# Optimization experiments

Hardware: AMD Instinct MI355X
Metric: run time of the kernel (lower is better)

Reference implementation:

```python
import jax, jax.numpy as jnp
import numpy as np

EPS = float(np.finfo(np.float32).eps)
NUM_PROP = 5          # config.model.num_prop
NUM_STEP_S2V = 3      # config.model.num_step_set2vec


def _gru_cell(x, h, wih, whh, bih, bhh):
    # PyTorch GRUCell: gate order r, z, n
    gi = x @ wih.T + bih
    gh = h @ whh.T + bhh
    ir, iz, in_ = jnp.split(gi, 3, axis=-1)
    hr, hz, hn = jnp.split(gh, 3, axis=-1)
    r = jax.nn.sigmoid(ir + hr)
    z = jax.nn.sigmoid(iz + hz)
    n = jnp.tanh(in_ + r * hn)
    return (1.0 - z) * n + z * h


def _lstm_cell(x, h, c, wih, whh, bih, bhh):
    # PyTorch LSTMCell: gate order i, f, g, o
    g = x @ wih.T + bih + h @ whh.T + bhh
    i, f, gg, o = jnp.split(g, 4, axis=-1)
    c2 = jax.nn.sigmoid(f) * c + jax.nn.sigmoid(i) * jnp.tanh(gg)
    return jax.nn.sigmoid(o) * jnp.tanh(c2), c2


def _set2vec(m, wih, whh, bih, bhh):
    # Set2Vec / set2set encoder (Vinyals et al. 2015) over a node set m: [N, H].
    # Returns q_star: [2H] = concat(LSTM hidden, attention read).
    H = m.shape[-1]
    h = jnp.zeros((H,), m.dtype)
    c = jnp.zeros((H,), m.dtype)
    q = jnp.zeros((2 * H,), m.dtype)
    for _ in range(NUM_STEP_S2V):
        h, c = _lstm_cell(q, h, c, wih, whh, bih, bhh)
        att = jax.nn.softmax(m @ h)   # [N] attention over set elements
        r = att @ m                   # [H] read vector
        q = jnp.concatenate([h, r])
    return q


def setup_inputs() -> dict:
    key = jax.random.key(0)
    ks = jax.random.split(key, 12)
    B, N, Da, Din, H, E1, Dout = 32, 512, 100, 64, 128, 4, 16
    s = 0.05
    return {
        "node_feat": jax.random.randint(ks[0], (B, N), 0, Da),
        "L": jax.random.randint(ks[1], (B, N, N, E1), 0, 2).astype(jnp.float32),
        "node_emb": jax.random.normal(ks[2], (Da, Din)) * s,
        "W_in": jax.random.normal(ks[3], (H, Din)) * s,
        "b_in": jnp.zeros((H,)),
        "edge_emb": jax.random.normal(ks[4], (E1, H * H)) * s,
        "gru_wih": jax.random.normal(ks[5], (3 * H, E1 * H)) * s,
        "gru_whh": jax.random.normal(ks[6], (3 * H, H)) * s,
        "gru_bih": jnp.zeros((3 * H,)),
        "gru_bhh": jnp.zeros((3 * H,)),
        "lstm_wih": jax.random.normal(ks[7], (4 * H, 2 * H)) * s,
        "lstm_whh": jax.random.normal(ks[8], (4 * H, H)) * s,
        "lstm_bih": jnp.zeros((4 * H,)),
        "lstm_bhh": jnp.zeros((4 * H,)),
        "W_out": jax.random.normal(ks[9], (Dout, 2 * H)) * s,
        "b_out": jnp.zeros((Dout,)),
    }


def reference(node_feat, L, node_emb, W_in, b_in, edge_emb,
              gru_wih, gru_whh, gru_bih, gru_bhh,
              lstm_wih, lstm_whh, lstm_bih, lstm_bhh,
              W_out, b_out):
    B, N = node_feat.shape
    H = W_in.shape[0]
    E1 = edge_emb.shape[0]
    # L[L != 0] = 1.0  (binarize adjacency)
    A = jnp.where(L != 0, 1.0, 0.0).astype(L.dtype)            # [B,N,N,E1]
    # node embedding + input linear
    state = node_emb[node_feat] @ W_in.T + b_in                # [B,N,H]
    Eop = edge_emb.reshape(E1, H, H)                           # per-edge-type operator
    for _ in range(NUM_PROP):
        # per-edge-type message: state @ edge_em  (all types at once)
        msg = jnp.einsum('bnh,ehk->bnek', state, Eop)          # [B,N,E1,H]
        # sum aggregation: bmm(A[...,e], msg_e)
        agg = jnp.einsum('bmne,bnek->bmek', A, msg)            # [B,N,E1,H]
        msg_cat = agg.reshape(B, N, E1 * H)                    # cat over edge types (dim=2)
        state = _gru_cell(msg_cat, state, gru_wih, gru_whh, gru_bih, gru_bhh)
        # dropout p=0.0 -> identity
    # Set2Vec per graph (mask=None path), then output linear
    q = jax.vmap(lambda s: _set2vec(s, lstm_wih, lstm_whh, lstm_bih, lstm_bhh))(state)  # [B,2H]
    return q @ W_out.T + b_out                                 # [B,Dout]
```

## Files before the change

### kernel.cpp

```cpp
#include <hip/hip_runtime.h>
#include <hip/hip_bf16.h>

#define BB 32
#define NN 512
#define DA 100
#define DIN 64
#define HH 128
#define E1 4
#define DOUT 16
#define NPROP 5
#define NS2V 3
#define MHALF 8192

typedef __attribute__((ext_vector_type(8))) short bf16x8;
typedef __attribute__((ext_vector_type(4))) float f32x4;
typedef __attribute__((ext_vector_type(4))) unsigned short us4;
typedef __attribute__((ext_vector_type(8))) unsigned short us8;
typedef unsigned short ushort_t;

__device__ __forceinline__ unsigned short f2bf(float f) {
    __hip_bfloat16 h = __float2bfloat16(f);
    return *reinterpret_cast<unsigned short*>(&h);
}
__device__ __forceinline__ float bf2f(unsigned short u) {
    unsigned v = ((unsigned)u) << 16;
    float f;
    __builtin_memcpy(&f, &v, 4);
    return f;
}

__device__ __forceinline__ void gload_lds16(const void* g, void* l) {
    __builtin_amdgcn_global_load_lds(
        (const __attribute__((address_space(1))) void*)g,
        (__attribute__((address_space(3))) void*)l, 16, 0, 0);
}

__global__ __launch_bounds__(256) void pack_A_kernel(const float* __restrict__ L,
                                                     unsigned* __restrict__ Abits) {
    int t = blockIdx.x * 256 + threadIdx.x;
    int n = t & (NN - 1);
    int m = (t >> 9) & (NN - 1);
    int b = t >> 18;
    float4 v = *reinterpret_cast<const float4*>(L + ((size_t)(b * NN + m) * NN + n) * E1);
    unsigned long long mk[E1];
    mk[0] = __ballot(v.x != 0.f);
    mk[1] = __ballot(v.y != 0.f);
    mk[2] = __ballot(v.z != 0.f);
    mk[3] = __ballot(v.w != 0.f);
    int lane = threadIdx.x & 63;
    if (lane < 8) {
        int e = lane >> 1, half = lane & 1;
        unsigned word = half ? (unsigned)(mk[e] >> 32) : (unsigned)mk[e];
        int wbase = (n >> 5) & ~1;
        Abits[((size_t)(b * E1 + e) * NN + m) * 16 + wbase + half] = word;
    }
}

__global__ void convW_kernel(const float* __restrict__ EE, const float* __restrict__ wih,
                             const float* __restrict__ whh,
                             ushort_t* __restrict__ U_h, ushort_t* __restrict__ U_l,
                             ushort_t* __restrict__ whh_h, ushort_t* __restrict__ whh_l) {
    int t = blockIdx.x * blockDim.x + threadIdx.x;
    if (t < 384 * 512) {
        int col = t & 511;
        int j = t >> 9;
        int e = col >> 7, h = col & 127;
        const float4* wp = reinterpret_cast<const float4*>(wih + (size_t)j * 512 + e * 128);
        const float4* ep = reinterpret_cast<const float4*>(EE + (size_t)e * 16384 + h * 128);
        float acc = 0.f;
        #pragma unroll 8
        for (int k4 = 0; k4 < 32; ++k4) {
            float4 a = wp[k4], b = ep[k4];
            acc = fmaf(a.x, b.x, fmaf(a.y, b.y, fmaf(a.z, b.z, fmaf(a.w, b.w, acc))));
        }
        unsigned short hi = f2bf(acc);
        U_h[t] = hi;
        U_l[t] = f2bf(acc - bf2f(hi));
        return;
    }
    int t2 = t - 384 * 512;
    if (t2 < 384 * 128) {
        float v = whh[t2];
        unsigned short hi = f2bf(v);
        whh_h[t2] = hi;
        whh_l[t2] = f2bf(v - bf2f(hi));
    }
}

__global__ void embed_kernel(const int* __restrict__ nf, const float* __restrict__ emb,
                             const float* __restrict__ Win, const float* __restrict__ bin,
                             ushort_t* __restrict__ s_hi, ushort_t* __restrict__ s_lo) {
    int row = blockIdx.x;
    int h = threadIdx.x;
    __shared__ float e[DIN];
    int a = nf[row];
    if (h < DIN) e[h] = emb[a * DIN + h];
    __syncthreads();
    float acc = bin[h];
    const float* w = Win + h * DIN;
    #pragma unroll
    for (int d = 0; d < DIN; ++d) acc = fmaf(e[d], w[d], acc);
    unsigned short hi = f2bf(acc);
    s_hi[row * HH + h] = hi;
    s_lo[row * HH + h] = f2bf(acc - bf2f(hi));
}

__global__ __launch_bounds__(256) void transpose_kernel(const ushort_t* __restrict__ src,
                                                        ushort_t* __restrict__ dst,
                                                        size_t splane) {
    __shared__ __align__(16) ushort_t tile[128][72];
    int row0 = blockIdx.x * 64;
    int tid = threadIdx.x;
    #pragma unroll
    for (int pl = 0; pl < 2; ++pl) {
        const ushort_t* s = src + pl * splane;
        ushort_t* d = dst + pl * splane;
        #pragma unroll
        for (int q = 0; q < 4; ++q) {
            int idx = q * 256 + tid;
            int r = idx >> 4, h8 = idx & 15;
            bf16x8 v = *reinterpret_cast<const bf16x8*>(s + (size_t)(row0 + r) * HH + h8 * 8);
            #pragma unroll
            for (int j = 0; j < 8; ++j) tile[h8 * 8 + j][r] = (ushort_t)v[j];
        }
        __syncthreads();
        {
            int h = tid >> 1, rseg = (tid & 1) * 32;
            #pragma unroll
            for (int s8 = 0; s8 < 4; ++s8) {
                us8 v = *reinterpret_cast<const us8*>(&tile[h][rseg + s8 * 8]);
                *reinterpret_cast<us8*>(&d[(size_t)h * 16384 + row0 + rseg + s8 * 8]) = v;
            }
        }
        __syncthreads();
    }
}

template <int MODE, bool AGG, bool XBITS, int K, bool XSPLIT, bool WSPLIT>
__global__ __launch_bounds__(256) void mm_kernel(const void* __restrict__ Xp, size_t xplane,
                                                 const ushort_t* __restrict__ W, size_t wplane,
                                                 const float* __restrict__ bias,
                                                 void* __restrict__ outv, size_t oplane,
                                                 int ldx, int ldw, int ldo) {
    __shared__ __align__(16) ushort_t Xs[2][128 * 32];
    __shared__ __align__(16) ushort_t Ws[2][64 * 32];
    int tid = threadIdx.x;
    int row0, col0;
    if constexpr (MODE == 3) {
        row0 = blockIdx.x * 128; col0 = blockIdx.y * 64;
    } else if constexpr (AGG) {
        row0 = (blockIdx.y & 3) * 128; col0 = (blockIdx.y >> 2) * 64;
    } else {
        row0 = blockIdx.y * 128; col0 = blockIdx.x * 64;
    }
    const ushort_t* X = (const ushort_t*)Xp;
    const unsigned* Xb = (const unsigned*)Xp;
    size_t out_off = 0;
    int wko = 0;
    if constexpr (AGG) {
        int bl = blockIdx.x, e = blockIdx.z;
        Xb += (size_t)(bl * E1 + e) * NN * 16;
        wko = bl * NN;
        out_off = (size_t)bl * NN * NN + (size_t)e * HH;
    }
    int lane = tid & 63;
    int wave = tid >> 6;
    int wm = wave & 1, wn = wave >> 1;
    int r16 = lane & 15, kg = lane >> 4;
    int lrow = lane >> 2;
    int lcol = (lane & 3) * 8;

    f32x4 acc[4][2] = {};

    for (int k0 = 0; k0 < K; k0 += 32) {
        unsigned xword;
        if constexpr (XBITS) {
            int m = tid >> 1;
            xword = Xb[(size_t)(row0 + m) * 16 + (k0 >> 5)];
        }
        __syncthreads();
        if constexpr (!XBITS) {
            #pragma unroll
            for (int q2 = 0; q2 < 2; ++q2) {
                int q = wave * 2 + q2;
                const ushort_t* g = X + (size_t)(row0 + q * 16 + lrow) * ldx + k0 + lcol;
                gload_lds16(g, &Xs[0][q * 512]);
                if constexpr (XSPLIT) gload_lds16(g + xplane, &Xs[1][q * 512]);
            }
        } else {
            int m = tid >> 1, sel = tid & 1;
            #pragma unroll
            for (int j8 = 0; j8 < 2; ++j8) {
                bf16x8 xv;
                #pragma unroll
                for (int j = 0; j < 8; ++j)
                    xv[j] = (short)(((xword >> (sel * 16 + j8 * 8 + j)) & 1u) ? 0x3F80 : 0);
                *reinterpret_cast<bf16x8*>(&Xs[0][m * 32 + sel * 16 + j8 * 8]) = xv;
            }
        }
        {
            const ushort_t* g = W + (size_t)(col0 + wave * 16 + lrow) * ldw + wko + k0 + lcol;
            gload_lds16(g, &Ws[0][wave * 512]);
            if constexpr (WSPLIT) gload_lds16(g + wplane, &Ws[1][wave * 512]);
        }
        __syncthreads();
        bf16x8 af_h[4], af_l[4], bf_h[2], bf_l[2];
        #pragma unroll
        for (int mi = 0; mi < 4; ++mi) {
            af_h[mi] = *reinterpret_cast<const bf16x8*>(&Xs[0][(wm * 64 + mi * 16 + r16) * 32 + kg * 8]);
            if constexpr (XSPLIT)
                af_l[mi] = *reinterpret_cast<const bf16x8*>(&Xs[1][(wm * 64 + mi * 16 + r16) * 32 + kg * 8]);
        }
        #pragma unroll
        for (int ni = 0; ni < 2; ++ni) {
            bf_h[ni] = *reinterpret_cast<const bf16x8*>(&Ws[0][(wn * 32 + ni * 16 + r16) * 32 + kg * 8]);
            if constexpr (WSPLIT)
                bf_l[ni] = *reinterpret_cast<const bf16x8*>(&Ws[1][(wn * 32 + ni * 16 + r16) * 32 + kg * 8]);
        }
        #pragma unroll
        for (int mi = 0; mi < 4; ++mi)
            #pragma unroll
            for (int ni = 0; ni < 2; ++ni) {
                acc[mi][ni] = __builtin_amdgcn_mfma_f32_16x16x32_bf16(af_h[mi], bf_h[ni], acc[mi][ni], 0, 0, 0);
                if constexpr (XSPLIT)
                    acc[mi][ni] = __builtin_amdgcn_mfma_f32_16x16x32_bf16(af_l[mi], bf_h[ni], acc[mi][ni], 0, 0, 0);
                if constexpr (WSPLIT)
                    acc[mi][ni] = __builtin_amdgcn_mfma_f32_16x16x32_bf16(af_h[mi], bf_l[ni], acc[mi][ni], 0, 0, 0);
            }
    }

    if constexpr (MODE == 3) {
        float* out = (float*)outv;
        #pragma unroll
        for (int ni = 0; ni < 2; ++ni) {
            int col = col0 + wn * 32 + ni * 16 + r16;
            float bv = bias[col];
            #pragma unroll
            for (int mi = 0; mi < 4; ++mi) {
                int rowb = row0 + wm * 64 + mi * 16 + kg * 4;
                #pragma unroll
                for (int j = 0; j < 4; ++j)
                    out[(size_t)(rowb + j) * ldo + col] = acc[mi][ni][j] + bv;
            }
        }
    } else {
        ushort_t* out = (ushort_t*)outv + out_off;
        #pragma unroll
        for (int ni = 0; ni < 2; ++ni) {
            int col = col0 + wn * 32 + ni * 16 + r16;
            #pragma unroll
            for (int mi = 0; mi < 4; ++mi) {
                int rowb = row0 + wm * 64 + mi * 16 + kg * 4;
                #pragma unroll
                for (int j = 0; j < 4; ++j) {
                    float v = acc[mi][ni][j];
                    unsigned short hv = f2bf(v);
                    out[(size_t)(rowb + j) * ldo + col] = hv;
                    out[oplane + (size_t)(rowb + j) * ldo + col] = f2bf(v - bf2f(hv));
                }
            }
        }
    }
}

__global__ void gru_gate_kernel(const float* __restrict__ gi, const float* __restrict__ gh,
                                ushort_t* __restrict__ s_hi, ushort_t* __restrict__ s_lo,
                                size_t half_off, int total) {
    int t = blockIdx.x * blockDim.x + threadIdx.x;
    if (t >= total) return;
    int row = t >> 7, j = t & 127;
    const float* gir = gi + (size_t)row * 384;
    const float* ghr = gh + (size_t)row * 384;
    float ir = gir[j], iz = gir[128 + j], in_ = gir[256 + j];
    float hr = ghr[j], hz = ghr[128 + j], hn = ghr[256 + j];
    float r = 1.f / (1.f + expf(-(ir + hr)));
    float z = 1.f / (1.f + expf(-(iz + hz)));
    float n = tanhf(in_ + r * hn);
    size_t g = half_off + (size_t)t;
    float h = bf2f(s_hi[g]) + bf2f(s_lo[g]);
    float v = (1.f - z) * n + z * h;
    unsigned short hv = f2bf(v);
    s_hi[g] = hv;
    s_lo[g] = f2bf(v - bf2f(hv));
}


__global__ __launch_bounds__(256) void s2v_g_kernel(int step,
        const float* __restrict__ hvec, const float* __restrict__ rpart,
        const float* __restrict__ wih, const float* __restrict__ whh,
        const float* __restrict__ bih, const float* __restrict__ bhh,
        float* __restrict__ g_all) {
    int b = blockIdx.y, tid = threadIdx.x;
    int j = blockIdx.x * 256 + tid;
    __shared__ float q[256];
    if (step > 0) {
        if (tid < 128) q[tid] = hvec[b * 128 + tid];
        else {
            int h2 = tid - 128;
            const float* rp = rpart + (size_t)b * 512;
            q[tid] = rp[h2] + rp[128 + h2] + rp[256 + h2] + rp[384 + h2];
        }
    } else {
        q[tid] = 0.f;
    }
    __syncthreads();
    float acc = bih[j] + bhh[j];
    if (step > 0) {
        const float4* wi = reinterpret_cast<const float4*>(wih + (size_t)j * 256);
        #pragma unroll 8
        for (int d4 = 0; d4 < 64; ++d4) {
            float4 w = wi[d4];
            acc = fmaf(q[d4 * 4 + 0], w.x, fmaf(q[d4 * 4 + 1], w.y,
                  fmaf(q[d4 * 4 + 2], w.z, fmaf(q[d4 * 4 + 3], w.w, acc))));
        }
        const float4* wp = reinterpret_cast<const float4*>(whh + (size_t)j * 128);
        #pragma unroll 8
        for (int d4 = 0; d4 < 32; ++d4) {
            float4 w = wp[d4];
            acc = fmaf(q[d4 * 4 + 0], w.x, fmaf(q[d4 * 4 + 1], w.y,
                  fmaf(q[d4 * 4 + 2], w.z, fmaf(q[d4 * 4 + 3], w.w, acc))));
        }
    }
    g_all[(size_t)b * 512 + j] = acc;
}

__global__ __launch_bounds__(256) void s2v_cl_kernel(int step,
        const float* __restrict__ g_all, float* __restrict__ cvec, float* __restrict__ hvec,
        const ushort_t* __restrict__ s_hi, const ushort_t* __restrict__ s_lo,
        float* __restrict__ logits) {
    int b = blockIdx.y, chunk = blockIdx.x, tid = threadIdx.x;
    __shared__ float hs[HH];
    if (tid < HH) {
        const float* g = g_all + (size_t)b * 512;
        float i_ = 1.f / (1.f + expf(-g[tid]));
        float f_ = 1.f / (1.f + expf(-g[128 + tid]));
        float g_ = tanhf(g[256 + tid]);
        float o_ = 1.f / (1.f + expf(-g[384 + tid]));
        float c0 = (step == 0) ? 0.f : cvec[b * 128 + tid];
        float c2 = f_ * c0 + i_ * g_;
        float hn = o_ * tanhf(c2);
        hs[tid] = hn;
        if (chunk == 0) { cvec[b * 128 + tid] = c2; hvec[b * 128 + tid] = hn; }
    }
    __syncthreads();
    int n = chunk * 256 + tid;
    const ushort_t* ph = s_hi + ((size_t)b * NN + n) * HH;
    const ushort_t* pl = s_lo + ((size_t)b * NN + n) * HH;
    float lg = 0.f;
    #pragma unroll
    for (int i8 = 0; i8 < 16; ++i8) {
        bf16x8 vh = *reinterpret_cast<const bf16x8*>(ph + i8 * 8);
        bf16x8 vl = *reinterpret_cast<const bf16x8*>(pl + i8 * 8);
        #pragma unroll
        for (int k = 0; k < 8; ++k)
            lg = fmaf(bf2f((ushort_t)vh[k]) + bf2f((ushort_t)vl[k]), hs[i8 * 8 + k], lg);
    }
    logits[(size_t)b * 512 + n] = lg;
}

__global__ __launch_bounds__(256) void s2v_read_kernel(const float* __restrict__ logits,
        const ushort_t* __restrict__ t_hi, const ushort_t* __restrict__ t_lo,
        float* __restrict__ rpart) {
    int b = blockIdx.y, chunk = blockIdx.x, tid = threadIdx.x;
    __shared__ float lgs[NN];
    __shared__ float att[128];
    __shared__ float wred[8];
    __shared__ float red[256];
    lgs[tid] = logits[(size_t)b * 512 + tid];
    lgs[256 + tid] = logits[(size_t)b * 512 + 256 + tid];
    __syncthreads();
    float mv = fmaxf(lgs[tid], lgs[tid + 256]);
    #pragma unroll
    for (int m = 32; m >= 1; m >>= 1) mv = fmaxf(mv, __shfl_xor(mv, m));
    if ((tid & 63) == 0) wred[tid >> 6] = mv;
    __syncthreads();
    float mx = fmaxf(fmaxf(wred[0], wred[1]), fmaxf(wred[2], wred[3]));
    float sv = expf(lgs[tid] - mx) + expf(lgs[tid + 256] - mx);
    #pragma unroll
    for (int m = 32; m >= 1; m >>= 1) sv += __shfl_xor(sv, m);
    if ((tid & 63) == 0) wred[4 + (tid >> 6)] = sv;
    __syncthreads();
    float inv = 1.f / (wred[4] + wred[5] + wred[6] + wred[7]);
    if (tid < 128) att[tid] = expf(lgs[chunk * 128 + tid] - mx) * inv;
    __syncthreads();
    int hh = tid & 127, half = tid >> 7;
    int colb = b * NN + chunk * 128 + half * 64;
    const ushort_t* ph = t_hi + (size_t)hh * 16384 + colb;
    const ushort_t* pl = t_lo + (size_t)hh * 16384 + colb;
    float racc = 0.f;
    #pragma unroll
    for (int i8 = 0; i8 < 8; ++i8) {
        bf16x8 vh = *reinterpret_cast<const bf16x8*>(ph + i8 * 8);
        bf16x8 vl = *reinterpret_cast<const bf16x8*>(pl + i8 * 8);
        #pragma unroll
        for (int k = 0; k < 8; ++k)
            racc = fmaf(att[half * 64 + i8 * 8 + k],
                        bf2f((ushort_t)vh[k]) + bf2f((ushort_t)vl[k]), racc);
    }
    red[tid] = racc;
    __syncthreads();
    if (tid < 128)
        rpart[(size_t)b * 512 + chunk * 128 + tid] = red[tid] + red[128 + tid];
}

__global__ __launch_bounds__(256) void s2v_out_kernel(const float* __restrict__ hvec,
        const float* __restrict__ rpart, const float* __restrict__ Wout,
        const float* __restrict__ bout, float* __restrict__ out) {
    int b = blockIdx.x, tid = threadIdx.x;
    __shared__ float q[256];
    if (tid < 128) q[tid] = hvec[b * 128 + tid];
    else {
        int h2 = tid - 128;
        const float* rp = rpart + (size_t)b * 512;
        q[tid] = rp[h2] + rp[128 + h2] + rp[256 + h2] + rp[384 + h2];
    }
    __syncthreads();
    if (tid < DOUT) {
        float acc = bout[tid];
        const float4* w = reinterpret_cast<const float4*>(Wout + (size_t)tid * 256);
        #pragma unroll 8
        for (int d4 = 0; d4 < 64; ++d4) {
            float4 wv = w[d4];
            acc = fmaf(q[d4 * 4 + 0], wv.x, fmaf(q[d4 * 4 + 1], wv.y,
                  fmaf(q[d4 * 4 + 2], wv.z, fmaf(q[d4 * 4 + 3], wv.w, acc))));
        }
        out[b * DOUT + tid] = acc;
    }
}

extern "C" void kernel_launch(void* const* d_in, const int* in_sizes, int n_in,
                              void* d_out, int out_size, void* d_ws, size_t ws_size,
                              hipStream_t stream) {
    const int*   node_feat = (const int*)d_in[0];
    const float* L         = (const float*)d_in[1];
    const float* node_emb  = (const float*)d_in[2];
    const float* W_in      = (const float*)d_in[3];
    const float* b_in      = (const float*)d_in[4];
    const float* edge_emb  = (const float*)d_in[5];
    const float* gru_wih   = (const float*)d_in[6];
    const float* gru_whh   = (const float*)d_in[7];
    const float* gru_bih   = (const float*)d_in[8];
    const float* gru_bhh   = (const float*)d_in[9];
    const float* lstm_wih  = (const float*)d_in[10];
    const float* lstm_whh  = (const float*)d_in[11];
    const float* lstm_bih  = (const float*)d_in[12];
    const float* lstm_bhh  = (const float*)d_in[13];
    const float* W_out     = (const float*)d_in[14];
    const float* b_out     = (const float*)d_in[15];
    float* out = (float*)d_out;

    char* ws = (char*)d_ws;
    const bool full = ws_size >= ((size_t)110 << 20);

    ushort_t* state_hi  = (ushort_t*)ws;
    ushort_t* stateT_hi = (ushort_t*)(ws + (8u << 20));
    unsigned* Abits     = (unsigned*)(ws + (16u << 20));
    ushort_t* S2        = (ushort_t*)(ws + (20u << 20));
    size_t s2plane      = full ? 8388608u : 4194304u;
    float*    gi        = (float*)(ws + (full ? (52ull << 20) : (36ull << 20)));
    float*    gh        = (float*)(ws + (full ? (76ull << 20) : (48ull << 20)));
    ushort_t* U_h       = (ushort_t*)(ws + (full ? (100ull << 20) : (60ull << 20)));
    ushort_t* U_l       = U_h + 196608;
    ushort_t* whh_h     = U_l + 196608;
    ushort_t* whh_l     = whh_h + 49152;
    float*    s2v       = (float*)(ws + (full ? (101ull << 20) : (61ull << 20)));
    float*    g_all     = s2v;
    float*    logits    = s2v + 16384;
    float*    hvec      = s2v + 32768;
    float*    cvec      = s2v + 36864;
    float*    rpart     = s2v + 40960;

    const size_t SPLANE = 2097152;

    pack_A_kernel<<<(BB * NN * NN) / 256, 256, 0, stream>>>(L, Abits);
    convW_kernel<<<(384 * 512 + 384 * 128) / 256, 256, 0, stream>>>(
        edge_emb, gru_wih, gru_whh, U_h, U_l, whh_h, whh_l);
    embed_kernel<<<BB * NN, 128, 0, stream>>>(node_feat, node_emb, W_in, b_in,
                                              state_hi, state_hi + SPLANE);

    const int nh     = full ? 1 : 2;
    const int graphs = full ? 32 : 16;
    const int ydim   = full ? 128 : 64;
    const int rows   = full ? 16384 : MHALF;

    for (int p = 0; p < NPROP; ++p) {
        transpose_kernel<<<256, 256, 0, stream>>>(state_hi, stateT_hi, SPLANE);
        for (int half = 0; half < nh; ++half) {
            const unsigned* Ab = Abits + (size_t)half * 16 * E1 * NN * 16;
            mm_kernel<4, true, true, 512, false, true><<<dim3(graphs, 8, 4), 256, 0, stream>>>(
                Ab, 0, stateT_hi + (size_t)half * MHALF, SPLANE, nullptr,
                S2, s2plane, 0, 16384, 512);
            mm_kernel<3, false, false, 512, true, true><<<dim3(ydim, 6), 256, 0, stream>>>(
                S2, s2plane, U_h, 196608, gru_bih, gi, 0, 512, 512, 384);
            mm_kernel<3, false, false, 128, true, true><<<dim3(ydim, 6), 256, 0, stream>>>(
                state_hi + (size_t)half * MHALF * HH, SPLANE, whh_h, 49152, gru_bhh,
                gh, 0, 128, 128, 384);
            gru_gate_kernel<<<(rows * HH) / 256, 256, 0, stream>>>(
                gi, gh, state_hi, state_hi + SPLANE,
                (size_t)half * MHALF * HH, rows * HH);
        }
    }
    transpose_kernel<<<256, 256, 0, stream>>>(state_hi, stateT_hi, SPLANE);

    for (int step = 0; step < NS2V; ++step) {
        s2v_g_kernel<<<dim3(2, BB), 256, 0, stream>>>(step, hvec, rpart,
                                                      lstm_wih, lstm_whh, lstm_bih, lstm_bhh,
                                                      g_all);
        s2v_cl_kernel<<<dim3(2, BB), 256, 0, stream>>>(step, g_all, cvec, hvec,
                                                       state_hi, state_hi + SPLANE, logits);
        s2v_read_kernel<<<dim3(4, BB), 256, 0, stream>>>(logits, stateT_hi,
                                                         stateT_hi + SPLANE, rpart);
    }
    s2v_out_kernel<<<BB, 256, 0, stream>>>(hvec, rpart, W_out, b_out, out);
}
```

Measured before the change: 581.1 us.

## Double GEMM K-step to 64 with XOR-swizzled LDS layout

The shared GEMM kernel now stages 64-wide K slices per iteration instead of 32, halving the number of barrier pairs and global-to-LDS rounds. The LDS tiles use an XOR swizzle on 16-byte slots to avoid bank conflicts on the MFMA fragment reads. LDS allocation is sized only for the split planes actually used. It assumes K is a multiple of 64, and the bit-expanded adjacency path now reads one 32-bit word per thread-half.

```diff
diff --git a/kernel.cpp b/kernel.cpp
--- a/kernel.cpp
+++ b/kernel.cpp
@@ -142,8 +142,10 @@
                                                  const float* __restrict__ bias,
                                                  void* __restrict__ outv, size_t oplane,
                                                  int ldx, int ldw, int ldo) {
-    __shared__ __align__(16) ushort_t Xs[2][128 * 32];
-    __shared__ __align__(16) ushort_t Ws[2][64 * 32];
+    constexpr int XP = XSPLIT ? 2 : 1;
+    constexpr int WP = WSPLIT ? 2 : 1;
+    __shared__ __align__(16) ushort_t Xs[XP][128 * 64];
+    __shared__ __align__(16) ushort_t Ws[WP][64 * 64];
     int tid = threadIdx.x;
     int row0, col0;
     if constexpr (MODE == 3) {
@@ -167,66 +169,81 @@
     int wave = tid >> 6;
     int wm = wave & 1, wn = wave >> 1;
     int r16 = lane & 15, kg = lane >> 4;
-    int lrow = lane >> 2;
-    int lcol = (lane & 3) * 8;
+    int lrow = lane >> 3;
+    int lslot = lane & 7;
 
     f32x4 acc[4][2] = {};
 
-    for (int k0 = 0; k0 < K; k0 += 32) {
-        unsigned xword;
+    for (int k0 = 0; k0 < K; k0 += 64) {
+        unsigned xw0;
         if constexpr (XBITS) {
-            int m = tid >> 1;
-            xword = Xb[(size_t)(row0 + m) * 16 + (k0 >> 5)];
+            int m = tid >> 1, sel = tid & 1;
+            xw0 = Xb[(size_t)(row0 + m) * 16 + (k0 >> 5) + sel];
         }
         __syncthreads();
         if constexpr (!XBITS) {
             #pragma unroll
-            for (int q2 = 0; q2 < 2; ++q2) {
-                int q = wave * 2 + q2;
-                const ushort_t* g = X + (size_t)(row0 + q * 16 + lrow) * ldx + k0 + lcol;
+            for (int q2 = 0; q2 < 4; ++q2) {
+                int q = wave * 4 + q2;
+                const ushort_t* g = X + (size_t)(row0 + q * 8 + lrow) * ldx + k0
+                                      + ((lslot ^ lrow) * 8);
                 gload_lds16(g, &Xs[0][q * 512]);
                 if constexpr (XSPLIT) gload_lds16(g + xplane, &Xs[1][q * 512]);
             }
         } else {
             int m = tid >> 1, sel = tid & 1;
             #pragma unroll
-            for (int j8 = 0; j8 < 2; ++j8) {
+            for (int j8 = 0; j8 < 4; ++j8) {
                 bf16x8 xv;
                 #pragma unroll
                 for (int j = 0; j < 8; ++j)
-                    xv[j] = (short)(((xword >> (sel * 16 + j8 * 8 + j)) & 1u) ? 0x3F80 : 0);
-                *reinterpret_cast<bf16x8*>(&Xs[0][m * 32 + sel * 16 + j8 * 8]) = xv;
+                    xv[j] = (short)(((xw0 >> (j8 * 8 + j)) & 1u) ? 0x3F80 : 0);
+                *reinterpret_cast<bf16x8*>(
+                    &Xs[0][m * 64 + (((sel << 2) + j8) ^ (m & 7)) * 8]) = xv;
             }
         }
         {
-            const ushort_t* g = W + (size_t)(col0 + wave * 16 + lrow) * ldw + wko + k0 + lcol;
-            gload_lds16(g, &Ws[0][wave * 512]);
-            if constexpr (WSPLIT) gload_lds16(g + wplane, &Ws[1][wave * 512]);
+            #pragma unroll
+            for (int q2 = 0; q2 < 2; ++q2) {
+                int q = wave * 2 + q2;
+                const ushort_t* g = W + (size_t)(col0 + q * 8 + lrow) * ldw + wko + k0
+                                      + ((lslot ^ lrow) * 8);
+                gload_lds16(g, &Ws[0][q * 512]);
+                if constexpr (WSPLIT) gload_lds16(g + wplane, &Ws[1][q * 512]);
+            }
         }
         __syncthreads();
-        bf16x8 af_h[4], af_l[4], bf_h[2], bf_l[2];
         #pragma unroll
-        for (int mi = 0; mi < 4; ++mi) {
-            af_h[mi] = *reinterpret_cast<const bf16x8*>(&Xs[0][(wm * 64 + mi * 16 + r16) * 32 + kg * 8]);
-            if constexpr (XSPLIT)
-                af_l[mi] = *reinterpret_cast<const bf16x8*>(&Xs[1][(wm * 64 + mi * 16 + r16) * 32 + kg * 8]);
-        }
-        #pragma unroll
-        for (int ni = 0; ni < 2; ++ni) {
-            bf_h[ni] = *reinterpret_cast<const bf16x8*>(&Ws[0][(wn * 32 + ni * 16 + r16) * 32 + kg * 8]);
-            if constexpr (WSPLIT)
-                bf_l[ni] = *reinterpret_cast<const bf16x8*>(&Ws[1][(wn * 32 + ni * 16 + r16) * 32 + kg * 8]);
-        }
-        #pragma unroll
-        for (int mi = 0; mi < 4; ++mi)
+        for (int kk = 0; kk < 2; ++kk) {
+            int sbase = kg + kk * 4;
+            bf16x8 af_h[4], af_l[4], bf_h[2], bf_l[2];
+            #pragma unroll
+            for (int mi = 0; mi < 4; ++mi) {
+                int r = wm * 64 + mi * 16 + r16;
+                int off = r * 64 + (sbase ^ (r & 7)) * 8;
+                af_h[mi] = *reinterpret_cast<const bf16x8*>(&Xs[0][off]);
+                if constexpr (XSPLIT)
+                    af_l[mi] = *reinterpret_cast<const bf16x8*>(&Xs[XP - 1][off]);
+            }
             #pragma unroll
             for (int ni = 0; ni < 2; ++ni) {
-                acc[mi][ni] = __builtin_amdgcn_mfma_f32_16x16x32_bf16(af_h[mi], bf_h[ni], acc[mi][ni], 0, 0, 0);
-                if constexpr (XSPLIT)
-                    acc[mi][ni] = __builtin_amdgcn_mfma_f32_16x16x32_bf16(af_l[mi], bf_h[ni], acc[mi][ni], 0, 0, 0);
+                int r = wn * 32 + ni * 16 + r16;
+                int off = r * 64 + (sbase ^ (r & 7)) * 8;
+                bf_h[ni] = *reinterpret_cast<const bf16x8*>(&Ws[0][off]);
                 if constexpr (WSPLIT)
-                    acc[mi][ni] = __builtin_amdgcn_mfma_f32_16x16x32_bf16(af_h[mi], bf_l[ni], acc[mi][ni], 0, 0, 0);
-            }
+                    bf_l[ni] = *reinterpret_cast<const bf16x8*>(&Ws[WP - 1][off]);
+            }
+            #pragma unroll
+            for (int mi = 0; mi < 4; ++mi)
+                #pragma unroll
+                for (int ni = 0; ni < 2; ++ni) {
+                    acc[mi][ni] = __builtin_amdgcn_mfma_f32_16x16x32_bf16(af_h[mi], bf_h[ni], acc[mi][ni], 0, 0, 0);
+                    if constexpr (XSPLIT)
+                        acc[mi][ni] = __builtin_amdgcn_mfma_f32_16x16x32_bf16(af_l[mi], bf_h[ni], acc[mi][ni], 0, 0, 0);
+                    if constexpr (WSPLIT)
+                        acc[mi][ni] = __builtin_amdgcn_mfma_f32_16x16x32_bf16(af_h[mi], bf_l[ni], acc[mi][ni], 0, 0, 0);
+                }
+        }
     }
 
     if constexpr (MODE == 3) {
```

Measured after the change: 573.5 us (median of 2 runs). About the same (-1.3%).

## Double-buffer LDS tiles in mm_kernel and XOR-swizzle layout to avoid bank conflicts

Applied to the files above, without the earlier changes.

Restructures the GEMM main loop to stage the next K-slice into a second LDS buffer while the current one feeds MFMAs, removing one barrier per iteration and overlapping global-to-LDS loads with compute. It also XOR-swizzles the 8-element column slot by row index on both store and load to reduce LDS bank conflicts on the fragment reads. The cost is double the LDS footprint for split variants, which may lower occupancy. The swizzle must match across the async gload_lds writes and the reads.

```diff
diff --git a/kernel.cpp b/kernel.cpp
--- a/kernel.cpp
+++ b/kernel.cpp
@@ -142,8 +142,10 @@
                                                  const float* __restrict__ bias,
                                                  void* __restrict__ outv, size_t oplane,
                                                  int ldx, int ldw, int ldo) {
-    __shared__ __align__(16) ushort_t Xs[2][128 * 32];
-    __shared__ __align__(16) ushort_t Ws[2][64 * 32];
+    constexpr int XP = XSPLIT ? 2 : 1;
+    constexpr int WP = WSPLIT ? 2 : 1;
+    __shared__ __align__(16) ushort_t Xs[2][XP][128 * 32];
+    __shared__ __align__(16) ushort_t Ws[2][WP][64 * 32];
     int tid = threadIdx.x;
     int row0, col0;
     if constexpr (MODE == 3) {
@@ -168,54 +170,62 @@
     int wm = wave & 1, wn = wave >> 1;
     int r16 = lane & 15, kg = lane >> 4;
     int lrow = lane >> 2;
-    int lcol = (lane & 3) * 8;
+    int lslot = lane & 3;
 
     f32x4 acc[4][2] = {};
 
-    for (int k0 = 0; k0 < K; k0 += 32) {
-        unsigned xword;
-        if constexpr (XBITS) {
-            int m = tid >> 1;
-            xword = Xb[(size_t)(row0 + m) * 16 + (k0 >> 5)];
-        }
-        __syncthreads();
+    auto stage = [&](int buf, int k0) {
         if constexpr (!XBITS) {
             #pragma unroll
             for (int q2 = 0; q2 < 2; ++q2) {
                 int q = wave * 2 + q2;
-                const ushort_t* g = X + (size_t)(row0 + q * 16 + lrow) * ldx + k0 + lcol;
-                gload_lds16(g, &Xs[0][q * 512]);
-                if constexpr (XSPLIT) gload_lds16(g + xplane, &Xs[1][q * 512]);
+                const ushort_t* g = X + (size_t)(row0 + q * 16 + lrow) * ldx + k0
+                                      + ((lslot ^ (lrow & 3)) * 8);
+                gload_lds16(g, &Xs[buf][0][q * 512]);
+                if constexpr (XSPLIT) gload_lds16(g + xplane, &Xs[buf][1][q * 512]);
             }
         } else {
             int m = tid >> 1, sel = tid & 1;
+            unsigned xw = Xb[(size_t)(row0 + m) * 16 + (k0 >> 5)];
             #pragma unroll
             for (int j8 = 0; j8 < 2; ++j8) {
                 bf16x8 xv;
                 #pragma unroll
                 for (int j = 0; j < 8; ++j)
-                    xv[j] = (short)(((xword >> (sel * 16 + j8 * 8 + j)) & 1u) ? 0x3F80 : 0);
-                *reinterpret_cast<bf16x8*>(&Xs[0][m * 32 + sel * 16 + j8 * 8]) = xv;
+                    xv[j] = (short)(((xw >> (sel * 16 + j8 * 8 + j)) & 1u) ? 0x3F80 : 0);
+                int slot = (sel * 2 + j8) ^ (m & 3);
+                *reinterpret_cast<bf16x8*>(&Xs[buf][0][m * 32 + slot * 8]) = xv;
             }
         }
         {
-            const ushort_t* g = W + (size_t)(col0 + wave * 16 + lrow) * ldw + wko + k0 + lcol;
-            gload_lds16(g, &Ws[0][wave * 512]);
-            if constexpr (WSPLIT) gload_lds16(g + wplane, &Ws[1][wave * 512]);
-        }
+            const ushort_t* g = W + (size_t)(col0 + wave * 16 + lrow) * ldw + wko + k0
+                                  + ((lslot ^ (lrow & 3)) * 8);
+            gload_lds16(g, &Ws[buf][0][wave * 512]);
+            if constexpr (WSPLIT) gload_lds16(g + wplane, &Ws[buf][1][wave * 512]);
+        }
+    };
+
+    stage(0, 0);
+    int cur = 0;
+    for (int k0 = 0; k0 < K; k0 += 32) {
         __syncthreads();
+        if (k0 + 32 < K) stage(cur ^ 1, k0 + 32);
         bf16x8 af_h[4], af_l[4], bf_h[2], bf_l[2];
         #pragma unroll
         for (int mi = 0; mi < 4; ++mi) {
-            af_h[mi] = *reinterpret_cast<const bf16x8*>(&Xs[0][(wm * 64 + mi * 16 + r16) * 32 + kg * 8]);
+            int r = wm * 64 + mi * 16 + r16;
+            int off = r * 32 + ((kg ^ (r16 & 3)) * 8);
+            af_h[mi] = *reinterpret_cast<const bf16x8*>(&Xs[cur][0][off]);
             if constexpr (XSPLIT)
-                af_l[mi] = *reinterpret_cast<const bf16x8*>(&Xs[1][(wm * 64 + mi * 16 + r16) * 32 + kg * 8]);
+                af_l[mi] = *reinterpret_cast<const bf16x8*>(&Xs[cur][XP - 1][off]);
         }
         #pragma unroll
         for (int ni = 0; ni < 2; ++ni) {
-            bf_h[ni] = *reinterpret_cast<const bf16x8*>(&Ws[0][(wn * 32 + ni * 16 + r16) * 32 + kg * 8]);
+            int r = wn * 32 + ni * 16 + r16;
+            int off = r * 32 + ((kg ^ (r16 & 3)) * 8);
+            bf_h[ni] = *reinterpret_cast<const bf16x8*>(&Ws[cur][0][off]);
             if constexpr (WSPLIT)
-                bf_l[ni] = *reinterpret_cast<const bf16x8*>(&Ws[1][(wn * 32 + ni * 16 + r16) * 32 + kg * 8]);
+                bf_l[ni] = *reinterpret_cast<const bf16x8*>(&Ws[cur][WP - 1][off]);
         }
         #pragma unroll
         for (int mi = 0; mi < 4; ++mi)
@@ -227,6 +237,7 @@
                 if constexpr (WSPLIT)
                     acc[mi][ni] = __builtin_amdgcn_mfma_f32_16x16x32_bf16(af_h[mi], bf_l[ni], acc[mi][ni], 0, 0, 0);
             }
+        cur ^= 1;
     }
 
     if constexpr (MODE == 3) {
```

New measurement: 580.6 us. About the same (-0.1%).
